# Kernel tuning notes

Hardware: AMD Instinct MI355X
Metric: run time of the kernel (lower is better)

Reference implementation:

```python
import jax, jax.numpy as jnp
import numpy as np

N = 8192      # nodes
E = 131072    # global edges
SDIM = 256    # scalar channels
VDIM = 64     # vector channels
EDIM = 128    # edge feature dim
L = 5         # num_layers
DIN = 2 * SDIM + EDIM + 4        # [s_src, s_tgt, e, d, a, |p_src|, |p_tgt|]
DOUT = SDIM + 2 * VDIM + 1 + EDIM  # [m_s, w_v1, w_v2, w_p, e_new]
HID = SDIM


def setup_inputs() -> dict:
    key = jax.random.key(0)
    ks = jax.random.split(key, 12)
    s = jax.random.normal(ks[0], (N, SDIM), jnp.float32)
    v = 0.1 * jax.random.normal(ks[1], (N, 3, VDIM), jnp.float32)
    p = 3.0 * jax.random.normal(ks[2], (N, 3), jnp.float32)
    e = jax.random.normal(ks[3], (E, EDIM), jnp.float32)
    edge_index = jax.random.randint(ks[4], (2, E), 0, N, dtype=jnp.int32)
    W1 = jax.random.normal(ks[5], (L, DIN, HID), jnp.float32) / np.sqrt(DIN)
    W2 = jax.random.normal(ks[6], (L, HID, DOUT), jnp.float32) / np.sqrt(HID)
    U1 = jax.random.normal(ks[7], (L, SDIM, SDIM), jnp.float32) / np.sqrt(SDIM)
    U2 = jax.random.normal(ks[8], (L, SDIM, SDIM), jnp.float32) / np.sqrt(SDIM)
    return {
        's': s, 'v': v, 'p': p, 'e': e, 'edge_index': edge_index,
        'ln_g': jnp.ones((L, SDIM), jnp.float32),
        'ln_b': jnp.zeros((L, SDIM), jnp.float32),
        'W1': W1, 'b1': jnp.zeros((L, HID), jnp.float32),
        'W2': W2, 'b2': jnp.zeros((L, DOUT), jnp.float32),
        'U1': U1, 'bU1': jnp.zeros((L, SDIM), jnp.float32),
        'U2': U2, 'bU2': jnp.zeros((L, SDIM), jnp.float32),
    }


def _edge_attrs(edge_index, pos):
    # Faithful to calculate_edge_attrs (sqrt=True, no ligand-pocket branch)
    src, tgt = edge_index[0], edge_index[1]
    r = pos[tgt] - pos[src]                                   # [E,3]
    a = jnp.sum(pos[tgt] * pos[src], axis=-1)                 # [E]
    d = jnp.sqrt(jnp.clip(jnp.sum(r * r, axis=-1), 1e-6, None))
    r_norm = r / (1.0 + d[:, None])
    return d, a, r_norm


def reference(s, v, p, e, edge_index, ln_g, ln_b, W1, b1, W2, b2, U1, bU1, U2, bU2):
    src, tgt = edge_index[0], edge_index[1]
    d, a, rn = _edge_attrs(edge_index, p)
    # in-degree counts for 'mean' vector/position aggregation
    cnt = jnp.clip(jax.ops.segment_sum(jnp.ones((E,), s.dtype), tgt, num_segments=N), 1.0)
    for i in range(L):
        # LayerNorm on scalar channels (vectors passed through)
        mu = jnp.mean(s, axis=-1, keepdims=True)
        var = jnp.mean((s - mu) ** 2, axis=-1, keepdims=True)
        s_ln = ln_g[i] * (s - mu) * jax.lax.rsqrt(var + 1e-5) + ln_b[i]
        pn = jnp.linalg.norm(p, axis=-1, keepdims=True)       # use_pos_norm features
        # gather-compute edge messages
        feat = jnp.concatenate(
            [s_ln[src], s_ln[tgt], e, d[:, None], a[:, None], pn[src], pn[tgt]], axis=-1)
        h = jax.nn.silu(feat @ W1[i] + b1[i])                 # [E,HID]
        out = h @ W2[i] + b2[i]                               # [E,DOUT]
        m_s = out[:, :SDIM]
        wv1 = out[:, SDIM:SDIM + VDIM]
        wv2 = out[:, SDIM + VDIM:SDIM + 2 * VDIM]
        wp = out[:, SDIM + 2 * VDIM:SDIM + 2 * VDIM + 1]
        e_new = out[:, SDIM + 2 * VDIM + 1:]
        has_v = 0.0 if i == 0 else 1.0                        # has_v_in = (i > 0)
        m_v = has_v * wv1[:, None, :] * v[src] + wv2[:, None, :] * rn[:, :, None]  # [E,3,VDIM]
        m_p = jnp.tanh(wp) * rn                               # [E,3]
        # scatter-aggregate (sum for scalars, mean for vectors/positions)
        s = s + jax.ops.segment_sum(m_s, tgt, num_segments=N)
        v = v + jax.ops.segment_sum(m_v, tgt, num_segments=N) / cnt[:, None, None]
        p = p + jax.ops.segment_sum(m_p, tgt, num_segments=N) / cnt[:, None]
        if i < L - 1:                                         # use_mlp_update = (i < num_layers - 1)
            s = s + jax.nn.silu(s @ U1[i] + bU1[i]) @ U2[i] + bU2[i]
        e = jax.nn.silu(e_new)
        # recompute_edge_attributes=True: redo gather/distance math on new positions
        d, a, rn = _edge_attrs(edge_index, p)
    return s, v, e, p
```

## Files before the change

### kernel.cpp

```cpp
#include <hip/hip_runtime.h>
#include <hip/hip_bf16.h>

namespace {

constexpr int NN   = 8192;
constexpr int NE   = 131072;
constexpr int SD   = 256;
constexpr int ED   = 128;
constexpr int NL   = 5;
constexpr int DINc = 644;
constexpr int KE   = 160;
constexpr int TE   = 5;
constexpr int T2   = 8;
constexpr int DOUTc= 513;
constexpr int HIDc = 256;

typedef __bf16 bf16x8 __attribute__((ext_vector_type(8)));
typedef float  f32x4  __attribute__((ext_vector_type(4)));

__device__ __forceinline__ float siluf(float x) { return x / (1.0f + __expf(-x)); }

__device__ __forceinline__ void gl_lds16(const void* gsrc, void* lds_uniform_base) {
  __builtin_amdgcn_global_load_lds(
      (const __attribute__((address_space(1))) unsigned int*)gsrc,
      (__attribute__((address_space(3))) unsigned int*)lds_uniform_base, 16, 0, 0);
}

__device__ __forceinline__ void wait_vm4() {
  asm volatile("s_waitcnt vmcnt(4)" ::: "memory");
  __builtin_amdgcn_sched_barrier(0);
}
__device__ __forceinline__ void wait_vm0() {
  asm volatile("s_waitcnt vmcnt(0)" ::: "memory");
  __builtin_amdgcn_sched_barrier(0);
}

__device__ __host__ __forceinline__ int swz(int kc) { return (kc * 5) & 7; }
__device__ __forceinline__ int apos(int kc, int row) { return kc * 64  + (row ^ swz(kc)); }
__device__ __forceinline__ int bpos(int kc, int n)   { return kc * 256 + (n   ^ swz(kc)); }

enum { MODE_H = 0, MODE_SADD = 2, MODE_SADD2 = 3, MODE_LIN = 4 };
enum { SRC_BF16 = 1, SRC_F32 = 2 };

struct GemmArgs {
  const __hip_bfloat16* Wt;
  const float* bias;
  const __hip_bfloat16* Abf;
  const float* Af32;
  __hip_bfloat16* bf_out;
  float* s_out;
  const int* rawcnt;
  const __hip_bfloat16* Wtb;
  const float* biasb;
  __hip_bfloat16* bf_outb;
  int dual;
};

__device__ __forceinline__ uint4 cvt8f(const float* p) {
  alignas(16) __hip_bfloat16 t8[8];
#pragma unroll
  for (int i = 0; i < 8; i++) t8[i] = __float2bfloat16(p[i]);
  return *(const uint4*)t8;
}

__device__ __forceinline__ float dot8u(const uint4& a, const __hip_bfloat16* w) {
  const __hip_bfloat16* ap = (const __hip_bfloat16*)&a;
  float s = 0.f;
#pragma unroll
  for (int j = 0; j < 8; j++) s += __bfloat162float(ap[j]) * __bfloat162float(w[j]);
  return s;
}

template<int MODE, int SRC, int KTOT, int BM>
__global__ __launch_bounds__(256) void gemm_k(GemmArgs g) {
  constexpr int T = KTOT / 32;
  constexpr int NC = KTOT / 8;
  constexpr int RPT = 256 / BM;
  constexpr int RMASK = RPT - 1;
  __shared__ alignas(16) unsigned short Apan[NC * BM * 8];
  __shared__ alignas(16) unsigned short Bsh[2][4 * 256 * 8];
  const int tid = threadIdx.x, lane = tid & 63, wave = tid >> 6;
  const int l16 = lane & 15, lhi = lane >> 4;
  const __hip_bfloat16* wtp = g.Wt;
  const float* biasp = g.bias;
  __hip_bfloat16* outp = g.bf_out;
  int blk = blockIdx.x;
  if constexpr (MODE == MODE_LIN) {
    const int half = gridDim.x >> 1;
    if (g.dual && blk >= half) { blk -= half; wtp = g.Wtb; biasp = g.biasb; outp = g.bf_outb; }
  }
  const int row0 = blk * BM;
  const int ar = tid / RPT, aq = tid % RPT;
  const int arow = row0 + ar;
  f32x4 acc[BM / 16][4] = {};

  auto issueB = [&](int t, int buf) {
    const __hip_bfloat16* src = wtp + (size_t)t * 1024 * 8;
    unsigned short* dst = &Bsh[buf][0];
#pragma unroll
    for (int i = 0; i < 4; i++)
      gl_lds16(src + (size_t)(i * 256 + wave * 64 + lane) * 8, dst + (i * 256 + wave * 64) * 8);
  };

  issueB(0, 0);
#pragma unroll
  for (int j = 0; j < NC / RPT; j++) {
    const int c = j * RPT + aq;
    uint4 o;
    if constexpr (SRC == SRC_BF16) o = *(const uint4*)(g.Abf + (size_t)arow * KTOT + c * 8);
    else                           o = cvt8f(g.Af32 + (size_t)arow * KTOT + c * 8);
    *(uint4*)&Apan[(c * BM + (ar ^ swz(aq))) * 8] = o;
  }
  __syncthreads();

  int cur = 0;
  for (int t = 0; t < T; ++t) {
    if (t + 1 < T) { issueB(t + 1, cur ^ 1); wait_vm4(); }
    else           { wait_vm0(); }
    bf16x8 bfr[4];
#pragma unroll
    for (int f = 0; f < 4; f++)
      bfr[f] = *(const bf16x8*)&Bsh[cur][bpos(lhi, wave * 64 + f * 16 + l16) * 8];
#pragma unroll
    for (int fr = 0; fr < BM / 16; fr++) {
      const int kc = t * 4 + lhi;
      const bf16x8 afr = *(const bf16x8*)&Apan[(kc * BM + ((fr * 16 + l16) ^ swz(kc & RMASK))) * 8];
#pragma unroll
      for (int fc = 0; fc < 4; fc++)
        acc[fr][fc] = __builtin_amdgcn_mfma_f32_16x16x32_bf16(afr, bfr[fc], acc[fr][fc], 0, 0, 0);
    }
    cur ^= 1;
  }

#pragma unroll
  for (int fr = 0; fr < BM / 16; fr++) {
#pragma unroll
    for (int fc = 0; fc < 4; fc++) {
      const int n = wave * 64 + fc * 16 + l16;
#pragma unroll
      for (int r = 0; r < 4; r++) {
        const int row = row0 + fr * 16 + lhi * 4 + r;
        const float valf = acc[fr][fc][r];
        if constexpr (MODE == MODE_H) {
          outp[(size_t)row * HIDc + n] = __float2bfloat16(siluf(valf + biasp[n]));
        } else if constexpr (MODE == MODE_LIN) {
          outp[(size_t)row * HIDc + n] = __float2bfloat16(valf + biasp[n]);
        } else if constexpr (MODE == MODE_SADD) {
          const float rc = (float)g.rawcnt[row];
          g.s_out[(size_t)row * SD + n] += valf + rc * biasp[n];
        } else {
          g.s_out[(size_t)row * SD + n] += valf + biasp[n];
        }
      }
    }
  }
}

struct FusedArgs {
  const __hip_bfloat16* W1e;
  const __hip_bfloat16* W2s;
  const float* b2L;
  const int* src; const int* tgt;
  const int* rank;
  const __hip_bfloat16* e_bf;
  const __hip_bfloat16* tail;
  const __hip_bfloat16* p1;
  const __hip_bfloat16* p2;
  const __hip_bfloat16* w384;
  const float* rn;
  float* mp;
  __hip_bfloat16* h_out;
  __hip_bfloat16* wv_out;
  __hip_bfloat16* e_bf_out;
  float* e_f32_out;
  int write_e_f32;
};

__global__ __launch_bounds__(256) void fused_k(FusedArgs g) {
  __shared__ alignas(16) unsigned short Ash[4 * 64 * 8];
  __shared__ alignas(16) unsigned short Bsh[2][4 * 256 * 8];
  __shared__ alignas(16) unsigned short Hsh[32 * 64 * 8];
  __shared__ float wps[4][64];
  __shared__ int Rk[64];
  const int tid = threadIdx.x, lane = tid & 63, wave = tid >> 6;
  const int l16 = lane & 15, lhi = lane >> 4;
  const int row0 = blockIdx.x * 64;
  const int ar = tid >> 2, aq = tid & 3;
  const int arow = row0 + ar;
  const int sn = g.src[arow], tn = g.tgt[arow];

  auto issueW = [&](const __hip_bfloat16* W, int t, int buf) {
    const __hip_bfloat16* src = W + (size_t)t * 1024 * 8;
    unsigned short* dst = &Bsh[buf][0];
#pragma unroll
    for (int i = 0; i < 4; i++)
      gl_lds16(src + (size_t)(i * 256 + wave * 64 + lane) * 8, dst + (i * 256 + wave * 64) * 8);
  };
  auto loadA = [&](int t, uint4& o) {
    const int kq = t * 32 + aq * 8;
    if (kq < 128) o = *(const uint4*)(g.e_bf + (size_t)arow * ED + kq);
    else          o = *(const uint4*)(g.tail + (size_t)arow * 32 + (kq - 128));
  };

  uint4 a;
  loadA(0, a);
  issueW(g.W1e, 0, 0);
  if (tid < 64) Rk[tid] = g.rank[row0 + tid];

#pragma unroll
  for (int j = 0; j < 8; j++) {
    const int c = j * 4 + aq;
    uint4 r1 = *(const uint4*)(g.p1 + (size_t)sn * SD + c * 8);
    uint4 r2 = *(const uint4*)(g.p2 + (size_t)tn * SD + c * 8);
    const __hip_bfloat16* h1 = (const __hip_bfloat16*)&r1;
    const __hip_bfloat16* h2 = (const __hip_bfloat16*)&r2;
    alignas(16) __hip_bfloat16 o8[8];
#pragma unroll
    for (int m = 0; m < 8; m++)
      o8[m] = __float2bfloat16(__bfloat162float(h1[m]) + __bfloat162float(h2[m]));
    *(uint4*)&Hsh[(c * 64 + (ar ^ swz(aq))) * 8] = *(const uint4*)o8;
  }

  f32x4 acc1[4][4] = {};
  int cur = 0;
  for (int t = 0; t < TE; ++t) {
    *(uint4*)&Ash[apos(aq, ar) * 8] = a;
    __syncthreads();
    if (t + 1 < TE) { issueW(g.W1e, t + 1, cur ^ 1); loadA(t + 1, a); }
    bf16x8 wfr[4], efr[4];
#pragma unroll
    for (int f = 0; f < 4; f++) {
      wfr[f] = *(const bf16x8*)&Bsh[cur][bpos(lhi, wave * 64 + f * 16 + l16) * 8];
      efr[f] = *(const bf16x8*)&Ash[apos(lhi, f * 16 + l16) * 8];
    }
#pragma unroll
    for (int fr = 0; fr < 4; fr++)
#pragma unroll
      for (int fc = 0; fc < 4; fc++)
        acc1[fr][fc] = __builtin_amdgcn_mfma_f32_16x16x32_bf16(wfr[fr], efr[fc], acc1[fr][fc], 0, 0, 0);
    __syncthreads();
    cur ^= 1;
  }

  issueW(g.W2s, 0, 0);

  float pw[4] = {0.f, 0.f, 0.f, 0.f};
#pragma unroll
  for (int fr = 0; fr < 4; fr++) {
    const int nb = wave * 64 + fr * 16 + lhi * 4;
    const int kc = nb >> 3, off = nb & 7;
    uint2 wr = *(const uint2*)(g.w384 + nb);
    const __hip_bfloat16* w4 = (const __hip_bfloat16*)&wr;
#pragma unroll
    for (int fc = 0; fc < 4; fc++) {
      const int row = fc * 16 + l16;
      unsigned short* slot = &Hsh[(kc * 64 + (row ^ swz(kc & 3))) * 8 + off];
      uint2 pr = *(const uint2*)slot;
      const __hip_bfloat16* pp = (const __hip_bfloat16*)&pr;
      alignas(8) __hip_bfloat16 hb[4];
#pragma unroll
      for (int r = 0; r < 4; r++) {
        const float hv = siluf(acc1[fr][fc][r] + __bfloat162float(pp[r]));
        hb[r] = __float2bfloat16(hv);
        pw[fc] += hv * __bfloat162float(w4[r]);
      }
      *(uint2*)slot = *(const uint2*)hb;
      *(uint2*)(g.h_out + (size_t)Rk[row] * HIDc + nb) = *(const uint2*)hb;
    }
  }

#pragma unroll
  for (int fc = 0; fc < 4; fc++) {
    pw[fc] += __shfl_xor(pw[fc], 16);
    pw[fc] += __shfl_xor(pw[fc], 32);
  }
  if (lane < 16) {
#pragma unroll
    for (int fc = 0; fc < 4; fc++) wps[wave][fc * 16 + lane] = pw[fc];
  }
  __syncthreads();
  if (tid < 64) {
    const float s = wps[0][tid] + wps[1][tid] + wps[2][tid] + wps[3][tid];
    const float wpt = tanhf(s + g.b2L[384]);
    const int rk = Rk[tid];
#pragma unroll
    for (int c = 0; c < 3; c++)
      g.mp[(size_t)rk * 3 + c] = wpt * g.rn[(size_t)(row0 + tid) * 3 + c];
  }

  f32x4 acc2[4][4] = {};
  cur = 0;
  for (int t = 0; t < T2; ++t) {
    if (t + 1 < T2) { issueW(g.W2s, t + 1, cur ^ 1); wait_vm4(); }
    else            { wait_vm0(); }
    bf16x8 afr[4], bfr[4];
#pragma unroll
    for (int f = 0; f < 4; f++) {
      const int kc = t * 4 + lhi;
      afr[f] = *(const bf16x8*)&Hsh[(kc * 64 + ((f * 16 + l16) ^ swz(lhi))) * 8];
      bfr[f] = *(const bf16x8*)&Bsh[cur][bpos(lhi, wave * 64 + f * 16 + l16) * 8];
    }
#pragma unroll
    for (int fr = 0; fr < 4; fr++)
#pragma unroll
      for (int fc = 0; fc < 4; fc++)
        acc2[fr][fc] = __builtin_amdgcn_mfma_f32_16x16x32_bf16(afr[fr], bfr[fc], acc2[fr][fc], 0, 0, 0);
    cur ^= 1;
  }

#pragma unroll
  for (int fr = 0; fr < 4; fr++) {
#pragma unroll
    for (int fc = 0; fc < 4; fc++) {
      const int n = wave * 64 + fc * 16 + l16;
#pragma unroll
      for (int r = 0; r < 4; r++) {
        const int lr = fr * 16 + lhi * 4 + r;
        const int row = row0 + lr;
        const float valf = acc2[fr][fc][r];
        if (n < 128) {
          g.wv_out[(size_t)Rk[lr] * 128 + n] = __float2bfloat16(valf + g.b2L[256 + n]);
        } else {
          const float sv = siluf(valf + g.b2L[257 + n]);
          g.e_bf_out[(size_t)row * ED + (n - 128)] = __float2bfloat16(sv);
          if (g.write_e_f32) g.e_f32_out[(size_t)row * ED + (n - 128)] = sv;
        }
      }
    }
  }
}

__global__ __launch_bounds__(256) void ln_k(const float* __restrict__ s,
                                            const float* __restrict__ gl, const float* __restrict__ bl,
                                            __hip_bfloat16* __restrict__ s_ln) {
  const int wave = threadIdx.x >> 6, lane = threadIdx.x & 63;
  const int node = blockIdx.x * 4 + wave;
  const float* srow = s + (size_t)node * SD;
  float x[4], sum = 0.f, sq = 0.f;
#pragma unroll
  for (int i = 0; i < 4; i++) { x[i] = srow[lane * 4 + i]; sum += x[i]; sq += x[i] * x[i]; }
#pragma unroll
  for (int off = 1; off < 64; off <<= 1) { sum += __shfl_xor(sum, off); sq += __shfl_xor(sq, off); }
  const float mu = sum * (1.0f / SD);
  const float var = sq * (1.0f / SD) - mu * mu;
  const float rstd = rsqrtf(var + 1e-5f);
#pragma unroll
  for (int i = 0; i < 4; i++) {
    const int c = lane * 4 + i;
    s_ln[(size_t)node * SD + c] = __float2bfloat16(gl[c] * (x[i] - mu) * rstd + bl[c]);
  }
}

__global__ void edge_attr_k(const float* __restrict__ p, const int* __restrict__ src, const int* __restrict__ tgt,
                            const int* __restrict__ rank,
                            float* __restrict__ rn, float* __restrict__ rnp,
                            __hip_bfloat16* __restrict__ tail) {
  const int e = blockIdx.x * blockDim.x + threadIdx.x;
  if (e >= NE) return;
  const int s_ = src[e], t_ = tgt[e];
  const float sx = p[s_ * 3], sy = p[s_ * 3 + 1], sz = p[s_ * 3 + 2];
  const float tx = p[t_ * 3], ty = p[t_ * 3 + 1], tz = p[t_ * 3 + 2];
  const float rx = tx - sx, ry = ty - sy, rz = tz - sz;
  const float a = tx * sx + ty * sy + tz * sz;
  const float rr = rx * rx + ry * ry + rz * rz;
  const float d = sqrtf(fmaxf(rr, 1e-6f));
  const float inv = 1.0f / (1.0f + d);
  const float r0 = rx * inv, r1 = ry * inv, r2 = rz * inv;
  rn[e * 3] = r0; rn[e * 3 + 1] = r1; rn[e * 3 + 2] = r2;
  const int rk = rank[e];
  rnp[rk * 3] = r0; rnp[rk * 3 + 1] = r1; rnp[rk * 3 + 2] = r2;
  alignas(16) __hip_bfloat16 t8[8];
  t8[0] = __float2bfloat16(d);
  t8[1] = __float2bfloat16(a);
  t8[2] = __float2bfloat16(sqrtf(sx * sx + sy * sy + sz * sz));
  t8[3] = __float2bfloat16(sqrtf(tx * tx + ty * ty + tz * tz));
  t8[4] = t8[5] = t8[6] = t8[7] = __float2bfloat16(0.0f);
  __hip_bfloat16* tp = tail + (size_t)e * 32;
  uint4 z; z.x = z.y = z.z = z.w = 0;
  *(uint4*)tp = *(const uint4*)t8;
  *(uint4*)(tp + 8) = z;
  *(uint4*)(tp + 16) = z;
  *(uint4*)(tp + 24) = z;
}

__global__ void cvt_e_k(const float* __restrict__ e, __hip_bfloat16* __restrict__ ebf) {
  const int i = blockIdx.x * blockDim.x + threadIdx.x;
  const float* p = e + (size_t)i * 8;
  alignas(16) __hip_bfloat16 t8[8];
#pragma unroll
  for (int j = 0; j < 8; j++) t8[j] = __float2bfloat16(p[j]);
  *(uint4*)(ebf + (size_t)i * 8) = *(const uint4*)t8;
}

__global__ void count_k(const int* __restrict__ tgt, int* __restrict__ rawcnt) {
  const int e = blockIdx.x * blockDim.x + threadIdx.x;
  if (e < NE) atomicAdd(&rawcnt[tgt[e]], 1);
}

__global__ __launch_bounds__(256) void scan_k(const int* __restrict__ rawcnt, int* __restrict__ off) {
  __shared__ int ts[256];
  const int tid = threadIdx.x;
  const int base = tid * 32;
  int local[32];
  int s = 0;
#pragma unroll
  for (int i = 0; i < 32; i++) { local[i] = s; s += rawcnt[base + i]; }
  ts[tid] = s;
  __syncthreads();
  if (tid == 0) {
    int acc = 0;
    for (int i = 0; i < 256; i++) { int t = ts[i]; ts[i] = acc; acc += t; }
    off[NN] = acc;
  }
  __syncthreads();
  const int pre = ts[tid];
#pragma unroll
  for (int i = 0; i < 32; i++) off[base + i] = pre + local[i];
}

__global__ void scatter_k(const int* __restrict__ tgt, const int* __restrict__ srcp,
                          const int* __restrict__ off,
                          int* __restrict__ cursor, int* __restrict__ rank, int* __restrict__ psrc) {
  const int e = blockIdx.x * blockDim.x + threadIdx.x;
  if (e < NE) {
    const int t = tgt[e];
    const int pos = off[t] + atomicAdd(&cursor[t], 1);
    rank[e] = pos;
    psrc[pos] = srcp[e];
  }
}

__global__ __launch_bounds__(256) void agg_k(const int* __restrict__ off, const int* __restrict__ psrc,
                                             const __hip_bfloat16* __restrict__ h,
                                             const __hip_bfloat16* __restrict__ wv,
                                             const float* __restrict__ mp,
                                             const float* __restrict__ rnp,
                                             const float* __restrict__ v_old,
                                             float* __restrict__ v_new,
                                             float* __restrict__ Hagg,
                                             float* __restrict__ p_o,
                                             int hasv) {
  const int n = blockIdx.x;
  const int c = threadIdx.x;
  const int e0 = off[n], e1 = off[n + 1];
  const int c3 = c >> 6, ln = c & 63;
  float hs = 0.f, vs = 0.f, ps = 0.f;
  int j = e0;
  for (; j + 2 <= e1; j += 2) {
    const float h0 = __bfloat162float(h[(size_t)j * HIDc + c]);
    const float h1 = __bfloat162float(h[(size_t)(j + 1) * HIDc + c]);
    hs += h0 + h1;
    if (c < 192) {
      const int s0 = psrc[j], s1 = psrc[j + 1];
      float m0 = __bfloat162float(wv[(size_t)j * 128 + 64 + ln]) * rnp[j * 3 + c3];
      float m1 = __bfloat162float(wv[(size_t)(j + 1) * 128 + 64 + ln]) * rnp[(j + 1) * 3 + c3];
      if (hasv) {
        m0 += __bfloat162float(wv[(size_t)j * 128 + ln]) * v_old[(size_t)s0 * 192 + c];
        m1 += __bfloat162float(wv[(size_t)(j + 1) * 128 + ln]) * v_old[(size_t)s1 * 192 + c];
      }
      vs += m0 + m1;
    } else if (c < 195) {
      ps += mp[j * 3 + (c - 192)] + mp[(j + 1) * 3 + (c - 192)];
    }
  }
  for (; j < e1; j++) {
    hs += __bfloat162float(h[(size_t)j * HIDc + c]);
    if (c < 192) {
      float mv = __bfloat162float(wv[(size_t)j * 128 + 64 + ln]) * rnp[j * 3 + c3];
      if (hasv) mv += __bfloat162float(wv[(size_t)j * 128 + ln]) * v_old[(size_t)psrc[j] * 192 + c];
      vs += mv;
    } else if (c < 195) {
      ps += mp[j * 3 + (c - 192)];
    }
  }
  Hagg[(size_t)n * HIDc + c] = hs;
  const float inv = 1.0f / fmaxf((float)(e1 - e0), 1.0f);
  if (c < 192)      v_new[(size_t)n * 192 + c] = v_old[(size_t)n * 192 + c] + vs * inv;
  else if (c < 195) p_o[n * 3 + (c - 192)]    += ps * inv;
}

__global__ void zero_k(float* __restrict__ ptr, int n) {
  const int i = blockIdx.x * blockDim.x + threadIdx.x;
  if (i < n) ptr[i] = 0.f;
}

__global__ void prep_w1abs_k(const float* __restrict__ W1, __hip_bfloat16* __restrict__ W1aS,
                             __hip_bfloat16* __restrict__ W1bS) {
  const int idx = blockIdx.x * blockDim.x + threadIdx.x;
  if (idx >= NL * T2 * 1024) return;
  const int p = idx & 1023, t = (idx >> 10) % T2, l = idx / (T2 * 1024);
  const int kc = p >> 8, n = (p & 255) ^ swz(kc);
  alignas(16) __hip_bfloat16 a8[8], b8[8];
#pragma unroll
  for (int j = 0; j < 8; j++) {
    const int k = t * 32 + kc * 8 + j;
    a8[j] = __float2bfloat16(W1[((size_t)l * DINc + k) * HIDc + n]);
    b8[j] = __float2bfloat16(W1[((size_t)l * DINc + 256 + k) * HIDc + n]);
  }
  *(uint4*)(W1aS + (size_t)idx * 8) = *(const uint4*)a8;
  *(uint4*)(W1bS + (size_t)idx * 8) = *(const uint4*)b8;
}

__global__ void prep_w1es_k(const float* __restrict__ W1, __hip_bfloat16* __restrict__ W1eS) {
  const int idx = blockIdx.x * blockDim.x + threadIdx.x;
  if (idx >= NL * TE * 1024) return;
  const int p = idx & 1023, t = (idx >> 10) % TE, l = idx / (TE * 1024);
  const int kc = p >> 8, n = (p & 255) ^ swz(kc);
  alignas(16) __hip_bfloat16 e8[8];
#pragma unroll
  for (int j = 0; j < 8; j++) {
    const int k = t * 32 + kc * 8 + j;
    const int row = (k < 128) ? (512 + k) : ((k < 132) ? (640 + (k - 128)) : -1);
    e8[j] = __float2bfloat16(row >= 0 ? W1[((size_t)l * DINc + row) * HIDc + n] : 0.f);
  }
  *(uint4*)(W1eS + (size_t)idx * 8) = *(const uint4*)e8;
}

__global__ void prep_w2s_k(const float* __restrict__ W2, __hip_bfloat16* __restrict__ W2sS,
                           __hip_bfloat16* __restrict__ W2aS) {
  const int idx = blockIdx.x * blockDim.x + threadIdx.x;
  if (idx >= NL * T2 * 1024) return;
  const int p = idx & 1023, t = (idx >> 10) & 7, l = idx >> 13;
  const int kc = p >> 8, n = (p & 255) ^ swz(kc);
  const float* W2l = W2 + (size_t)l * HIDc * DOUTc;
  const int cs = (n < 128) ? (256 + n) : (257 + n);
  alignas(16) __hip_bfloat16 s8[8], a8[8];
#pragma unroll
  for (int j = 0; j < 8; j++) {
    const int k = t * 32 + kc * 8 + j;
    s8[j] = __float2bfloat16(W2l[(size_t)k * DOUTc + cs]);
    a8[j] = __float2bfloat16(W2l[(size_t)k * DOUTc + n]);
  }
  *(uint4*)(W2sS + (size_t)idx * 8) = *(const uint4*)s8;
  *(uint4*)(W2aS + (size_t)idx * 8) = *(const uint4*)a8;
}

__global__ void prep_uts_k(const float* __restrict__ U1, const float* __restrict__ U2,
                           __hip_bfloat16* __restrict__ U1S, __hip_bfloat16* __restrict__ U2S) {
  const int idx = blockIdx.x * blockDim.x + threadIdx.x;
  if (idx >= NL * T2 * 1024) return;
  const int p = idx & 1023, t = (idx >> 10) & 7, l = idx >> 13;
  const int kc = p >> 8, n = (p & 255) ^ swz(kc);
  alignas(16) __hip_bfloat16 u1[8], u2[8];
#pragma unroll
  for (int j = 0; j < 8; j++) {
    const int k = t * 32 + kc * 8 + j;
    u1[j] = __float2bfloat16(U1[((size_t)l * HIDc + k) * HIDc + n]);
    u2[j] = __float2bfloat16(U2[((size_t)l * HIDc + k) * HIDc + n]);
  }
  *(uint4*)(U1S + (size_t)idx * 8) = *(const uint4*)u1;
  *(uint4*)(U2S + (size_t)idx * 8) = *(const uint4*)u2;
}

__global__ void prep_w384_k(const float* __restrict__ W2, __hip_bfloat16* __restrict__ w384) {
  const int idx = blockIdx.x * blockDim.x + threadIdx.x;
  if (idx >= NL * HIDc) return;
  const int k = idx & 255, l = idx >> 8;
  w384[idx] = __float2bfloat16(W2[((size_t)l * HIDc + k) * DOUTc + 384]);
}

}

extern "C" void kernel_launch(void* const* d_in, const int* in_sizes, int n_in,
                              void* d_out, int out_size, void* d_ws, size_t ws_size,
                              hipStream_t stream) {
  (void)in_sizes; (void)n_in; (void)out_size; (void)ws_size;
  const float* s_in = (const float*)d_in[0];
  const float* v_in = (const float*)d_in[1];
  const float* p_in = (const float*)d_in[2];
  const float* e_in = (const float*)d_in[3];
  const int*   ei   = (const int*)d_in[4];
  const float* ln_g = (const float*)d_in[5];
  const float* ln_b = (const float*)d_in[6];
  const float* W1   = (const float*)d_in[7];
  const float* b1   = (const float*)d_in[8];
  const float* W2   = (const float*)d_in[9];
  const float* b2   = (const float*)d_in[10];
  const float* U1   = (const float*)d_in[11];
  const float* bU1  = (const float*)d_in[12];
  const float* U2   = (const float*)d_in[13];
  const float* bU2  = (const float*)d_in[14];

  float* s_o = (float*)d_out;
  float* v_o = s_o + (size_t)NN * SD;
  float* e_o = v_o + (size_t)NN * 192;
  float* p_o = e_o + (size_t)NE * ED;

  const int* srcp = ei;
  const int* tgtp = ei + NE;

  char* wp = (char*)d_ws;
  auto alloc = [&](size_t bytes) -> char* {
    char* r = wp; wp += (bytes + 255) & ~(size_t)255; return r;
  };
  __hip_bfloat16* s_ln = (__hip_bfloat16*)alloc((size_t)NN * SD * 2);
  __hip_bfloat16* hbuf = (__hip_bfloat16*)alloc((size_t)NE * HIDc * 2);
  __hip_bfloat16* ebf  = (__hip_bfloat16*)alloc((size_t)NE * ED * 2);
  __hip_bfloat16* tbuf = (__hip_bfloat16*)alloc((size_t)NN * HIDc * 2);
  __hip_bfloat16* wvbuf= (__hip_bfloat16*)alloc((size_t)NE * 128 * 2);
  __hip_bfloat16* tailb= (__hip_bfloat16*)alloc((size_t)NE * 32 * 2);
  __hip_bfloat16* p1buf= (__hip_bfloat16*)alloc((size_t)NN * SD * 2);
  __hip_bfloat16* p2buf= (__hip_bfloat16*)alloc((size_t)NN * SD * 2);
  float* rnbuf = (float*)alloc((size_t)NE * 3 * 4);
  float* rnpbuf= (float*)alloc((size_t)NE * 3 * 4);
  float* Hagg  = (float*)alloc((size_t)NN * SD * 4);
  float* vprev = (float*)alloc((size_t)NN * 192 * 4);
  float* mpbuf = (float*)alloc((size_t)NE * 3 * 4);
  float* zerobias = (float*)alloc(256 * 4);
  int*   rawcnt= (int*)alloc((size_t)NN * 4);
  int*   offb  = (int*)alloc((size_t)(NN + 1) * 4);
  int*   cursor= (int*)alloc((size_t)NN * 4);
  int*   rankb = (int*)alloc((size_t)NE * 4);
  int*   psrcb = (int*)alloc((size_t)NE * 4);
  __hip_bfloat16* W1aS = (__hip_bfloat16*)alloc((size_t)NL * T2 * 1024 * 8 * 2);
  __hip_bfloat16* W1bS = (__hip_bfloat16*)alloc((size_t)NL * T2 * 1024 * 8 * 2);
  __hip_bfloat16* W1eS = (__hip_bfloat16*)alloc((size_t)NL * TE * 1024 * 8 * 2);
  __hip_bfloat16* W2sS = (__hip_bfloat16*)alloc((size_t)NL * T2 * 1024 * 8 * 2);
  __hip_bfloat16* W2aS = (__hip_bfloat16*)alloc((size_t)NL * T2 * 1024 * 8 * 2);
  __hip_bfloat16* U1S  = (__hip_bfloat16*)alloc((size_t)NL * T2 * 1024 * 8 * 2);
  __hip_bfloat16* U2S  = (__hip_bfloat16*)alloc((size_t)NL * T2 * 1024 * 8 * 2);
  __hip_bfloat16* w384 = (__hip_bfloat16*)alloc((size_t)NL * HIDc * 2);

  hipMemcpyAsync(s_o, s_in, (size_t)NN * SD * 4, hipMemcpyDeviceToDevice, stream);
  hipMemcpyAsync(vprev, v_in, (size_t)NN * 192 * 4, hipMemcpyDeviceToDevice, stream);
  hipMemcpyAsync(p_o, p_in, (size_t)NN * 3 * 4, hipMemcpyDeviceToDevice, stream);

  prep_w1abs_k<<<(NL * T2 * 1024 + 255) / 256, 256, 0, stream>>>(W1, W1aS, W1bS);
  prep_w1es_k<<<(NL * TE * 1024 + 255) / 256, 256, 0, stream>>>(W1, W1eS);
  prep_w2s_k<<<(NL * T2 * 1024 + 255) / 256, 256, 0, stream>>>(W2, W2sS, W2aS);
  prep_uts_k<<<(NL * T2 * 1024 + 255) / 256, 256, 0, stream>>>(U1, U2, U1S, U2S);
  prep_w384_k<<<(NL * HIDc + 255) / 256, 256, 0, stream>>>(W2, w384);
  cvt_e_k<<<NE * ED / 8 / 256, 256, 0, stream>>>(e_in, ebf);
  zero_k<<<1, 256, 0, stream>>>(zerobias, 256);

  zero_k<<<(NN + 255) / 256, 256, 0, stream>>>((float*)rawcnt, NN);
  zero_k<<<(NN + 255) / 256, 256, 0, stream>>>((float*)cursor, NN);
  count_k<<<NE / 256, 256, 0, stream>>>(tgtp, rawcnt);
  scan_k<<<1, 256, 0, stream>>>(rawcnt, offb);
  scatter_k<<<NE / 256, 256, 0, stream>>>(tgtp, srcp, offb, cursor, rankb, psrcb);

  for (int l = 0; l < NL; l++) {
    ln_k<<<NN / 4, 256, 0, stream>>>(s_o, ln_g + l * SD, ln_b + l * SD, s_ln);
    edge_attr_k<<<NE / 256, 256, 0, stream>>>(p_o, srcp, tgtp, rankb, rnbuf, rnpbuf, tailb);

    GemmArgs gp{};
    gp.Wt = W1aS + (size_t)l * T2 * 1024 * 8; gp.bias = b1 + l * HIDc; gp.bf_out = p1buf;
    gp.Wtb = W1bS + (size_t)l * T2 * 1024 * 8; gp.biasb = zerobias; gp.bf_outb = p2buf;
    gp.Abf = s_ln; gp.dual = 1;
    gemm_k<MODE_LIN, SRC_BF16, 256, 64><<<2 * NN / 64, 256, 0, stream>>>(gp);

    FusedArgs gf{};
    gf.W1e = W1eS + (size_t)l * TE * 1024 * 8;
    gf.W2s = W2sS + (size_t)l * T2 * 1024 * 8;
    gf.b2L = b2 + l * DOUTc;
    gf.src = srcp; gf.tgt = tgtp; gf.rank = rankb;
    gf.e_bf = ebf; gf.tail = tailb;
    gf.p1 = p1buf; gf.p2 = p2buf; gf.w384 = w384 + l * HIDc;
    gf.rn = rnbuf; gf.mp = mpbuf;
    gf.h_out = hbuf; gf.wv_out = wvbuf; gf.e_bf_out = ebf; gf.e_f32_out = e_o;
    gf.write_e_f32 = (l == NL - 1) ? 1 : 0;
    fused_k<<<NE / 64, 256, 0, stream>>>(gf);

    const float* vold = (l & 1) ? (const float*)v_o : (const float*)vprev;
    float* vnew = (l & 1) ? vprev : v_o;
    agg_k<<<NN, 256, 0, stream>>>(offb, psrcb, hbuf, wvbuf, mpbuf, rnpbuf,
                                  vold, vnew, Hagg, p_o, (l > 0) ? 1 : 0);

    GemmArgs g3{};
    g3.Wt = W2aS + (size_t)l * T2 * 1024 * 8; g3.bias = b2 + l * DOUTc;
    g3.Af32 = Hagg; g3.s_out = s_o; g3.rawcnt = rawcnt;
    gemm_k<MODE_SADD, SRC_F32, 256, 32><<<NN / 32, 256, 0, stream>>>(g3);

    if (l < NL - 1) {
      GemmArgs g4{};
      g4.Wt = U1S + (size_t)l * T2 * 1024 * 8; g4.bias = bU1 + l * HIDc;
      g4.Af32 = s_o; g4.bf_out = tbuf;
      gemm_k<MODE_H, SRC_F32, 256, 32><<<NN / 32, 256, 0, stream>>>(g4);

      GemmArgs g5{};
      g5.Wt = U2S + (size_t)l * T2 * 1024 * 8; g5.bias = bU2 + l * HIDc;
      g5.Abf = tbuf; g5.s_out = s_o;
      gemm_k<MODE_SADD2, SRC_BF16, 256, 32><<<NN / 32, 256, 0, stream>>>(g5);
    }
  }
}
```

Baseline: 1.148 ms.

## Fuse per-node W2 scalar GEMM and two-layer MLP update into one kernel

Replaces three separate node-level GEMM launches (aggregated-message projection, U1 with SiLU, U2 residual) with a single kernel. It keeps each 32-row tile of the updated scalar state in LDS as bf16 and chains the three matmuls through it. This removes the round trip of s_out and the temporary hidden buffer through global memory, plus two kernel launches per layer. In exchange it serializes three K-loops per block, with B-tile prefetch only overlapping across stages, and it uses the weights as the MFMA A operand in a transposed fragment layout.

Measured after the change: 1.092 ms. -4.9%, faster.

```diff
diff --git a/kernel.cpp b/kernel.cpp
--- a/kernel.cpp
+++ b/kernel.cpp
@@ -39,7 +39,7 @@
 __device__ __forceinline__ int apos(int kc, int row) { return kc * 64  + (row ^ swz(kc)); }
 __device__ __forceinline__ int bpos(int kc, int n)   { return kc * 256 + (n   ^ swz(kc)); }
 
-enum { MODE_H = 0, MODE_SADD = 2, MODE_SADD2 = 3, MODE_LIN = 4 };
+enum { MODE_LIN = 4 };
 enum { SRC_BF16 = 1, SRC_F32 = 2 };
 
 struct GemmArgs {
@@ -48,8 +48,6 @@
   const __hip_bfloat16* Abf;
   const float* Af32;
   __hip_bfloat16* bf_out;
-  float* s_out;
-  const int* rawcnt;
   const __hip_bfloat16* Wtb;
   const float* biasb;
   __hip_bfloat16* bf_outb;
@@ -61,14 +59,6 @@
 #pragma unroll
   for (int i = 0; i < 8; i++) t8[i] = __float2bfloat16(p[i]);
   return *(const uint4*)t8;
-}
-
-__device__ __forceinline__ float dot8u(const uint4& a, const __hip_bfloat16* w) {
-  const __hip_bfloat16* ap = (const __hip_bfloat16*)&a;
-  float s = 0.f;
-#pragma unroll
-  for (int j = 0; j < 8; j++) s += __bfloat162float(ap[j]) * __bfloat162float(w[j]);
-  return s;
 }
 
 template<int MODE, int SRC, int KTOT, int BM>
@@ -85,7 +75,7 @@
   const float* biasp = g.bias;
   __hip_bfloat16* outp = g.bf_out;
   int blk = blockIdx.x;
-  if constexpr (MODE == MODE_LIN) {
+  {
     const int half = gridDim.x >> 1;
     if (g.dual && blk >= half) { blk -= half; wtp = g.Wtb; biasp = g.biasb; outp = g.bf_outb; }
   }
@@ -140,18 +130,143 @@
 #pragma unroll
       for (int r = 0; r < 4; r++) {
         const int row = row0 + fr * 16 + lhi * 4 + r;
-        const float valf = acc[fr][fc][r];
-        if constexpr (MODE == MODE_H) {
-          outp[(size_t)row * HIDc + n] = __float2bfloat16(siluf(valf + biasp[n]));
-        } else if constexpr (MODE == MODE_LIN) {
-          outp[(size_t)row * HIDc + n] = __float2bfloat16(valf + biasp[n]);
-        } else if constexpr (MODE == MODE_SADD) {
-          const float rc = (float)g.rawcnt[row];
-          g.s_out[(size_t)row * SD + n] += valf + rc * biasp[n];
-        } else {
-          g.s_out[(size_t)row * SD + n] += valf + biasp[n];
-        }
+        outp[(size_t)row * HIDc + n] = __float2bfloat16(acc[fr][fc][r] + biasp[n]);
       }
+    }
+  }
+}
+
+struct Node3Args {
+  const __hip_bfloat16* W2a;
+  const __hip_bfloat16* U1s;
+  const __hip_bfloat16* U2s;
+  const float* b2L;
+  const float* bU1;
+  const float* bU2;
+  const float* Hagg;
+  const int* rawcnt;
+  float* s_out;
+};
+
+template<int LAST>
+__global__ __launch_bounds__(256) void node3_k(Node3Args g) {
+  constexpr int BM = 32, RPT = 8, NC = 32, T = 8;
+  __shared__ alignas(16) unsigned short Apan[NC * BM * 8];
+  __shared__ alignas(16) unsigned short Bsh[2][4 * 256 * 8];
+  const int tid = threadIdx.x, lane = tid & 63, wave = tid >> 6;
+  const int l16 = lane & 15, lhi = lane >> 4;
+  const int row0 = blockIdx.x * BM;
+  const int ar = tid >> 3, aq = tid & 7;
+
+  auto issueB = [&](const __hip_bfloat16* W, int t, int buf) {
+    const __hip_bfloat16* src = W + (size_t)t * 1024 * 8;
+    unsigned short* dst = &Bsh[buf][0];
+#pragma unroll
+    for (int i = 0; i < 4; i++)
+      gl_lds16(src + (size_t)(i * 256 + wave * 64 + lane) * 8, dst + (i * 256 + wave * 64) * 8);
+  };
+
+  f32x4 acc[4][2];
+  auto kloop = [&](const __hip_bfloat16* W) {
+#pragma unroll
+    for (int i = 0; i < 4; i++)
+#pragma unroll
+      for (int j = 0; j < 2; j++) acc[i][j] = f32x4{0.f, 0.f, 0.f, 0.f};
+    int cur = 0;
+    for (int t = 0; t < T; ++t) {
+      if (t + 1 < T) { issueB(W, t + 1, cur ^ 1); wait_vm4(); }
+      else           { wait_vm0(); }
+      bf16x8 wfr[4], afr[2];
+#pragma unroll
+      for (int f = 0; f < 4; f++)
+        wfr[f] = *(const bf16x8*)&Bsh[cur][bpos(lhi, wave * 64 + f * 16 + l16) * 8];
+#pragma unroll
+      for (int f = 0; f < 2; f++) {
+        const int kc = t * 4 + lhi;
+        afr[f] = *(const bf16x8*)&Apan[(kc * BM + ((f * 16 + l16) ^ swz(kc & 7))) * 8];
+      }
+#pragma unroll
+      for (int fr = 0; fr < 4; fr++)
+#pragma unroll
+        for (int fc = 0; fc < 2; fc++)
+          acc[fr][fc] = __builtin_amdgcn_mfma_f32_16x16x32_bf16(wfr[fr], afr[fc], acc[fr][fc], 0, 0, 0);
+      cur ^= 1;
+    }
+  };
+
+  issueB(g.W2a, 0, 0);
+#pragma unroll
+  for (int j = 0; j < NC / RPT; j++) {
+    const int c = j * RPT + aq;
+    uint4 o = cvt8f(g.Hagg + (size_t)(row0 + ar) * SD + c * 8);
+    *(uint4*)&Apan[(c * BM + (ar ^ swz(aq))) * 8] = o;
+  }
+  __syncthreads();
+
+  kloop(g.W2a);
+  __syncthreads();
+  if constexpr (!LAST) issueB(g.U1s, 0, 0);
+
+#pragma unroll
+  for (int fr = 0; fr < 4; fr++) {
+    const int nb = wave * 64 + fr * 16 + lhi * 4;
+    const int kc = nb >> 3, off = nb & 7;
+    const f32x4 b4 = *(const f32x4*)(g.b2L + nb);
+#pragma unroll
+    for (int fc = 0; fc < 2; fc++) {
+      const int row = fc * 16 + l16;
+      const float rc = (float)g.rawcnt[row0 + row];
+      float* sp = g.s_out + (size_t)(row0 + row) * SD + nb;
+      f32x4 sold = *(const f32x4*)sp;
+      alignas(8) __hip_bfloat16 hb[4];
+      f32x4 s1;
+#pragma unroll
+      for (int r = 0; r < 4; r++) {
+        s1[r] = sold[r] + acc[fr][fc][r] + rc * b4[r];
+        hb[r] = __float2bfloat16(s1[r]);
+      }
+      *(f32x4*)sp = s1;
+      if constexpr (!LAST)
+        *(uint2*)&Apan[(kc * BM + (row ^ swz(kc & 7))) * 8 + off] = *(const uint2*)hb;
+    }
+  }
+  if constexpr (LAST) return;
+
+  __syncthreads();
+
+  kloop(g.U1s);
+  __syncthreads();
+  issueB(g.U2s, 0, 0);
+#pragma unroll
+  for (int fr = 0; fr < 4; fr++) {
+    const int nb = wave * 64 + fr * 16 + lhi * 4;
+    const int kc = nb >> 3, off = nb & 7;
+    const f32x4 b4 = *(const f32x4*)(g.bU1 + nb);
+#pragma unroll
+    for (int fc = 0; fc < 2; fc++) {
+      const int row = fc * 16 + l16;
+      alignas(8) __hip_bfloat16 hb[4];
+#pragma unroll
+      for (int r = 0; r < 4; r++)
+        hb[r] = __float2bfloat16(siluf(acc[fr][fc][r] + b4[r]));
+      *(uint2*)&Apan[(kc * BM + (row ^ swz(kc & 7))) * 8 + off] = *(const uint2*)hb;
+    }
+  }
+  __syncthreads();
+
+  kloop(g.U2s);
+#pragma unroll
+  for (int fr = 0; fr < 4; fr++) {
+    const int nb = wave * 64 + fr * 16 + lhi * 4;
+    const f32x4 b4 = *(const f32x4*)(g.bU2 + nb);
+#pragma unroll
+    for (int fc = 0; fc < 2; fc++) {
+      const int row = fc * 16 + l16;
+      float* sp = g.s_out + (size_t)(row0 + row) * SD + nb;
+      f32x4 s1 = *(const f32x4*)sp;
+#pragma unroll
+      for (int r = 0; r < 4; r++) s1[r] += acc[fr][fc][r] + b4[r];
+      *(f32x4*)sp = s1;
     }
   }
 }
@@ -596,7 +711,6 @@
   __hip_bfloat16* s_ln = (__hip_bfloat16*)alloc((size_t)NN * SD * 2);
   __hip_bfloat16* hbuf = (__hip_bfloat16*)alloc((size_t)NE * HIDc * 2);
   __hip_bfloat16* ebf  = (__hip_bfloat16*)alloc((size_t)NE * ED * 2);
-  __hip_bfloat16* tbuf = (__hip_bfloat16*)alloc((size_t)NN * HIDc * 2);
   __hip_bfloat16* wvbuf= (__hip_bfloat16*)alloc((size_t)NE * 128 * 2);
   __hip_bfloat16* tailb= (__hip_bfloat16*)alloc((size_t)NE * 32 * 2);
   __hip_bfloat16* p1buf= (__hip_bfloat16*)alloc((size_t)NN * SD * 2);
@@ -666,21 +780,13 @@
     agg_k<<<NN, 256, 0, stream>>>(offb, psrcb, hbuf, wvbuf, mpbuf, rnpbuf,
                                   vold, vnew, Hagg, p_o, (l > 0) ? 1 : 0);
 
-    GemmArgs g3{};
-    g3.Wt = W2aS + (size_t)l * T2 * 1024 * 8; g3.bias = b2 + l * DOUTc;
-    g3.Af32 = Hagg; g3.s_out = s_o; g3.rawcnt = rawcnt;
-    gemm_k<MODE_SADD, SRC_F32, 256, 32><<<NN / 32, 256, 0, stream>>>(g3);
-
-    if (l < NL - 1) {
-      GemmArgs g4{};
-      g4.Wt = U1S + (size_t)l * T2 * 1024 * 8; g4.bias = bU1 + l * HIDc;
-      g4.Af32 = s_o; g4.bf_out = tbuf;
-      gemm_k<MODE_H, SRC_F32, 256, 32><<<NN / 32, 256, 0, stream>>>(g4);
-
-      GemmArgs g5{};
-      g5.Wt = U2S + (size_t)l * T2 * 1024 * 8; g5.bias = bU2 + l * HIDc;
-      g5.Abf = tbuf; g5.s_out = s_o;
-      gemm_k<MODE_SADD2, SRC_BF16, 256, 32><<<NN / 32, 256, 0, stream>>>(g5);
-    }
-  }
-}
+    Node3Args gn{};
+    gn.W2a = W2aS + (size_t)l * T2 * 1024 * 8;
+    gn.U1s = U1S + (size_t)l * T2 * 1024 * 8;
+    gn.U2s = U2S + (size_t)l * T2 * 1024 * 8;
+    gn.b2L = b2 + l * DOUTc; gn.bU1 = bU1 + l * HIDc; gn.bU2 = bU2 + l * HIDc;
+    gn.Hagg = Hagg; gn.rawcnt = rawcnt; gn.s_out = s_o;
+    if (l < NL - 1) node3_k<0><<<NN / 32, 256, 0, stream>>>(gn);
+    else            node3_k<1><<<NN / 32, 256, 0, stream>>>(gn);
+  }
+}
```
